# Kernel optimization log

Measured on AMD Instinct MI355X. Metric: run time of the kernel, lower is better.

## Reference

```python
import jax, jax.numpy as jnp
import numpy as np

TEMPLATE0 = 3  # template[0]: prefix prompt length, positions [t0, t0+count) are kept verbatim

def setup_inputs() -> dict:
    key = jax.random.key(0)
    ks = jax.random.split(key, 6)
    B, S, H, E = 16, 512, 768, 19
    scale = 1.0 / np.sqrt(H)
    return {
        "sequence_output": jax.random.normal(ks[0], (B, S, H), jnp.float32),
        "label_init": jax.random.normal(ks[1], (E, H), jnp.float32),
        "attn_w": jax.random.normal(ks[2], (H, H), jnp.float32) * scale,
        "attn_b": jax.random.normal(ks[3], (H,), jnp.float32) * scale,
        "fc_w": jax.random.normal(ks[4], (H,), jnp.float32) * scale,
        "counts": jax.random.randint(ks[5], (B,), 1, 400, jnp.int32),
    }

def reference(sequence_output, label_init, attn_w, attn_b, fc_w, counts):
    # Vectorized form of GPT2SoftmaxForNer_LE.add_label_embedding + attention
    B, S, H = sequence_output.shape
    # attn_linear: torch Linear -> x @ W^T + b
    x_attn = jnp.einsum('bsh,gh->bsg', sequence_output, attn_w) + attn_b  # [B,S,H]
    # att_features = label_embedding + expanded input state; e = tanh(...)
    e = jnp.tanh(x_attn[:, :, None, :] + label_init[None, None, :, :])  # [B,S,E,H]
    scores = jnp.einsum('bseh,h->bse', e, fc_w)  # fc: Linear(H,1,bias=False)
    attn_dist = jax.nn.softmax(scores, axis=-1)
    # (original renormalizes softmax by its sum; sum==1 so it is a no-op)
    ctx = jnp.einsum('bse,eh->bsh', attn_dist, label_init)
    out = ctx + sequence_output  # residual add
    # restore original embeddings at positions [t0, t0 + counts[b])
    pos = jnp.arange(S)[None, :]  # [1,S]
    keep = (pos >= TEMPLATE0) & (pos < counts[:, None] + TEMPLATE0)  # [B,S]
    return jnp.where(keep[:, :, None], sequence_output, out)
```

## Files before the change

### kernel.cpp

```cpp
#include <hip/hip_runtime.h>
#include <hip/hip_fp16.h>

typedef __bf16 bf16_t;
typedef __bf16 bf16x8 __attribute__((ext_vector_type(8)));
typedef _Float16 f16_t;
typedef _Float16 f16x8 __attribute__((ext_vector_type(8)));
typedef float  f32x4  __attribute__((ext_vector_type(4)));

#define B_ 16
#define S_ 512
#define H_ 768
#define E_ 19
#define T0 3
#define ROWS (B_*S_)
#define SCAL 2.8853900817779268f

#define WS_W_OFF  0
#define WS_W_SZ   (H_*H_*2)
#define WS_LS_OFF (WS_W_OFF + WS_W_SZ)
#define WS_LS_SZ  (E_*H_*2)
#define WS_XS_OFF (WS_LS_OFF + WS_LS_SZ)
#define WS_XS_SZ  (ROWS*H_*2)
#define WS_NEED   (WS_XS_OFF + WS_XS_SZ)
#define WS_AB_OFF WS_NEED
#define WS_AB_SZ  (ROWS*H_*2)
#define WS_NEED2  (WS_AB_OFF + WS_AB_SZ)

__device__ __forceinline__ f16_t h_exp2(f16_t x) {
  __half hx = __builtin_bit_cast(__half, x);
  return __builtin_bit_cast(f16_t, hexp2(hx));
}
__device__ __forceinline__ f16_t h_rcp(f16_t x) {
  __half hx = __builtin_bit_cast(__half, x);
  return __builtin_bit_cast(f16_t, hrcp(hx));
}

__global__ __launch_bounds__(256) void prep_kernel(
    const float* __restrict__ w, const float* __restrict__ lab,
    const float* __restrict__ attb, const float* __restrict__ seq,
    bf16_t* __restrict__ wbf, f16_t* __restrict__ lsg, bf16_t* __restrict__ abf) {
  int t = blockIdx.x*256 + threadIdx.x;
  int i = t*8;
  if (i < H_*H_) {
    float4 u = *(const float4*)(w + i);
    float4 v = *(const float4*)(w + i + 4);
    bf16x8 b;
    b[0]=(bf16_t)(u.x*SCAL); b[1]=(bf16_t)(u.y*SCAL); b[2]=(bf16_t)(u.z*SCAL); b[3]=(bf16_t)(u.w*SCAL);
    b[4]=(bf16_t)(v.x*SCAL); b[5]=(bf16_t)(v.y*SCAL); b[6]=(bf16_t)(v.z*SCAL); b[7]=(bf16_t)(v.w*SCAL);
    *(bf16x8*)(wbf + i) = b;
  }
  if (t < E_*H_) {
    int col = t % H_;
    lsg[t] = (f16_t)((lab[t] + attb[col]) * SCAL);
  }
  if (i < ROWS*H_) {
    float4 u = *(const float4*)(seq + i);
    float4 v = *(const float4*)(seq + i + 4);
    bf16x8 b;
    b[0]=(bf16_t)u.x; b[1]=(bf16_t)u.y; b[2]=(bf16_t)u.z; b[3]=(bf16_t)u.w;
    b[4]=(bf16_t)v.x; b[5]=(bf16_t)v.y; b[6]=(bf16_t)v.z; b[7]=(bf16_t)v.w;
    *(bf16x8*)(abf + i) = b;
  }
}

#define G_BM 128
#define G_BN 128
#define G_BK 64
#define G_NT 256
#define G_STEPS (H_/G_BK)

__global__ __launch_bounds__(G_NT, 2) void gemm_xs2(
    const bf16_t* __restrict__ abf, const float* __restrict__ attb,
    const bf16_t* __restrict__ wbf, f16_t* __restrict__ xs) {
  __shared__ __align__(16) unsigned char smem[32768];
  const int tid  = threadIdx.x;
  const int lane = tid & 63, wv = tid >> 6;
  const int bid  = blockIdx.x;
  const int wg   = (bid & 7)*48 + (bid >> 3);
  const int rt   = wg / 6, ct = wg % 6;
  const int arow0 = rt * G_BM;
  const int bcol0 = ct * G_BN;
  const int wr = wv >> 1, wc = wv & 1;
  const int ar = lane & 15, kg = lane >> 4;

  f32x4 acc[4][4] = {};

  auto stage = [&](int s) {
    const int k0 = s * G_BK;
    #pragma unroll
    for (int it = 0; it < 4; ++it) {
      int Lb  = (wv*4 + it) * 1024;
      int L   = Lb + lane*16;
      int row = L >> 7;
      int c   = (L >> 4) & 7;
      int cs  = c ^ (row & 7);
      const bf16_t* srcA = abf + (size_t)(arow0 + row)*H_ + k0 + cs*8;
      __builtin_amdgcn_global_load_lds(
          (const __attribute__((address_space(1))) void*)srcA,
          (__attribute__((address_space(3))) void*)(smem + Lb), 16, 0, 0);
      const bf16_t* srcB = wbf + (size_t)(bcol0 + row)*H_ + k0 + cs*8;
      __builtin_amdgcn_global_load_lds(
          (const __attribute__((address_space(1))) void*)srcB,
          (__attribute__((address_space(3))) void*)(smem + 16384 + Lb), 16, 0, 0);
    }
  };

  stage(0);
  #pragma unroll 1
  for (int s = 0; s < G_STEPS; ++s) {
    __syncthreads();
    #pragma unroll
    for (int ks = 0; ks < 2; ++ks) {
      bf16x8 af[4], bfr[4];
      #pragma unroll
      for (int mf = 0; mf < 4; ++mf) {
        int row = wr*64 + mf*16 + ar;
        int g2  = ks*4 + kg;
        af[mf] = *(const bf16x8*)(smem + row*128 + ((g2 ^ (row & 7)) << 4));
      }
      #pragma unroll
      for (int nf = 0; nf < 4; ++nf) {
        int row = wc*64 + nf*16 + ar;
        int g2  = ks*4 + kg;
        bfr[nf] = *(const bf16x8*)(smem + 16384 + row*128 + ((g2 ^ (row & 7)) << 4));
      }
      #pragma unroll
      for (int mf = 0; mf < 4; ++mf)
        #pragma unroll
        for (int nf = 0; nf < 4; ++nf)
          acc[mf][nf] = __builtin_amdgcn_mfma_f32_16x16x32_bf16(af[mf], bfr[nf], acc[mf][nf], 0,0,0);
    }
    __syncthreads();
    if (s + 1 < G_STEPS) stage(s + 1);
  }

  float bc[4];
  #pragma unroll
  for (int nf = 0; nf < 4; ++nf) bc[nf] = attb[bcol0 + wc*64 + nf*16 + ar] * SCAL;
  #pragma unroll
  for (int mf = 0; mf < 4; ++mf) {
    int rbase = arow0 + wr*64 + mf*16 + kg*4;
    #pragma unroll
    for (int nf = 0; nf < 4; ++nf) {
      int col = bcol0 + wc*64 + nf*16 + ar;
      #pragma unroll
      for (int i = 0; i < 4; ++i)
        xs[(size_t)(rbase + i)*H_ + col] = (f16_t)(acc[mf][nf][i] + bc[nf]);
    }
  }
}

#define K2_R   4
#define K2_PAD 1552
#define K2_SALL (K2_R*K2_PAD)
#define K2_PP   (K2_SALL + K2_R*20*4)
#define K2_LDS  (K2_PP + K2_R*20*4)
__global__ __launch_bounds__(256, 6) void score_ctx(
    const f16_t* __restrict__ xs, const f16_t* __restrict__ lsg,
    const float* __restrict__ fcw, const float* __restrict__ seq,
    const float* __restrict__ lab, const int* __restrict__ counts,
    float* __restrict__ out) {
  __shared__ __align__(16) unsigned char smem[K2_LDS];
  float* Sall = (float*)(smem + K2_SALL);
  float* Pp   = (float*)(smem + K2_PP);
  const int tid = threadIdx.x;
  const int r0  = blockIdx.x * K2_R;

  for (int i = tid; i < K2_R*(H_/8); i += 256) {
    int row = i / (H_/8), kv = i % (H_/8);
    f16x8 v = *(const f16x8*)(xs + (size_t)(r0 + row)*H_ + kv*8);
    *(f16x8*)(smem + row*K2_PAD + kv*16) = v;
  }
  __syncthreads();

  const int g = tid >> 4, k = tid & 15;
  const int r = g & 3, eq = g >> 2;
  const f16_t* xrow = (const f16_t*)(smem + r*K2_PAD + k*96);
  const int ebase = eq*5;
  const f16_t* lbase = lsg + ebase*H_ + k*48;
  const f16_t one = (f16_t)1.0f;

  float s[5] = {};
  #pragma unroll 1
  for (int c = 0; c < 6; ++c) {
    f16x8 xh = *(const f16x8*)(xrow + c*8);
    f32x4 f0 = *(const f32x4*)(fcw + k*48 + c*8);
    f32x4 f1 = *(const f32x4*)(fcw + k*48 + c*8 + 4);
    #pragma unroll
    for (int j = 0; j < 5; ++j) {
      if (j == 4 && eq == 3) continue;
      f16x8 lh = *(const f16x8*)(lbase + j*H_ + c*8);
      f16x8 a  = xh + lh;
      #pragma unroll
      for (int q = 0; q < 8; ++q) {
        f16_t t = h_exp2(a[q]);
        f16_t u = (f16_t)(t + one);
        f16_t rr = h_rcp(u);
        float fq = (q < 4) ? f0[q] : f1[q-4];
        s[j] += fq * (float)rr;
      }
    }
  }
  #pragma unroll
  for (int off = 1; off < 16; off <<= 1)
    #pragma unroll
    for (int j = 0; j < 5; ++j)
      s[j] += __shfl_xor(s[j], off, 64);
  if (k == 0) {
    #pragma unroll
    for (int j = 0; j < 5; ++j) {
      int e = ebase + j;
      if (e < E_) Sall[r*20 + e] = s[j];
    }
  }
  __syncthreads();

  if (tid < K2_R) {
    float s2[E_]; float mx = -1e30f;
    #pragma unroll
    for (int e = 0; e < E_; ++e) {
      float v = -2.0f * Sall[tid*20 + e];
      s2[e] = v; mx = fmaxf(mx, v);
    }
    float ssum = 0.f;
    #pragma unroll
    for (int e = 0; e < E_; ++e) {
      float pr = __builtin_amdgcn_exp2f((s2[e] - mx) * 1.4426950408889634f);
      s2[e] = pr; ssum += pr;
    }
    float rr = __builtin_amdgcn_rcpf(ssum);
    #pragma unroll
    for (int e = 0; e < E_; ++e) Pp[tid*20 + e] = s2[e]*rr;
  }
  __syncthreads();

  if (tid < 192) {
    f32x4 o4[K2_R] = {};
    #pragma unroll 1
    for (int e = 0; e < E_; ++e) {
      f32x4 la = *(const f32x4*)(lab + e*H_ + tid*4);
      #pragma unroll
      for (int rr2 = 0; rr2 < K2_R; ++rr2) {
        float pv = Pp[rr2*20 + e];
        o4[rr2] += pv * la;
      }
    }
    const int batch = r0 >> 9;
    const int cnt = counts[batch];
    #pragma unroll
    for (int rr2 = 0; rr2 < K2_R; ++rr2) {
      int row = r0 + rr2;
      int sp  = row & 511;
      bool keep = (sp >= T0) && (sp < cnt + T0);
      size_t idx = (size_t)row*H_ + tid*4;
      f32x4 sv = *(const f32x4*)(seq + idx);
      f32x4 ov = keep ? sv : (sv + o4[rr2]);
      *(f32x4*)(out + idx) = ov;
    }
  }
}

#define BM 16
#define NW 6
#define NT (NW*64)
#define A_SZ   (BM*H_*2)
#define LS_OFF A_SZ
#define LS_SZ  (E_*H_*2)
#define LDS_SZ (A_SZ + LS_SZ)
#define SP_OFF 0
#define PP_OFF (NW*BM*20*4)

__global__ __launch_bounds__(NT, 3) void ner_fused(
    const float* __restrict__ seq, const float* __restrict__ lab,
    const float* __restrict__ attw, const float* __restrict__ attb,
    const float* __restrict__ fcw, const int* __restrict__ counts,
    float* __restrict__ out)
{
  __shared__ __align__(16) unsigned char smem[LDS_SZ];
  _Float16* Lsh = (_Float16*)(smem + LS_OFF);
  float* Sp = (float*)(smem + SP_OFF);
  float* Pp = (float*)(smem + PP_OFF);
  const int tid   = threadIdx.x;
  const int blk   = blockIdx.x;
  const int batch = blk >> 5;
  const int s0    = (blk & 31) * BM;
  const size_t rowbase = ((size_t)batch * S_ + s0) * H_;
  {
    const float4* src = (const float4*)(seq + rowbase);
    #pragma unroll
    for (int i = 0; i < (BM*H_/8)/NT; ++i) {
      int idx = i*NT + tid;
      int row = idx / (H_/8);
      int kv  = idx % (H_/8);
      float4 u = src[row*(H_/4) + kv*2];
      float4 v = src[row*(H_/4) + kv*2 + 1];
      bf16x8 b;
      b[0]=(bf16_t)u.x; b[1]=(bf16_t)u.y; b[2]=(bf16_t)u.z; b[3]=(bf16_t)u.w;
      b[4]=(bf16_t)v.x; b[5]=(bf16_t)v.y; b[6]=(bf16_t)v.z; b[7]=(bf16_t)v.w;
      int byte = row*(H_*2) + kv*16;
      *(bf16x8*)(smem + (byte ^ ((row & 7) << 4))) = b;
    }
  }
  for (int i = tid*4; i < E_*H_; i += NT*4) {
    int c = i % H_;
    float4 l4 = *(const float4*)(lab + i);
    float4 b4 = *(const float4*)(attb + c);
    int e = i / H_;
    #pragma unroll
    for (int j = 0; j < 4; ++j) {
      int col = c + j;
      int wv2 = col >> 7, rr = col & 127, n = rr >> 4, arr = rr & 15;
      float v = ((&l4.x)[j] + (&b4.x)[j]) * SCAL;
      Lsh[((e*NW + wv2)*16 + arr)*8 + n] = (_Float16)v;
    }
  }
  __syncthreads();
  const int lane = tid & 63;
  const int wv   = tid >> 6;
  const int ar   = lane & 15;
  const int kg   = lane >> 4;
  const int wbase = wv * (H_/NW);
  f32x4 acc[8] = {};
  {
    const int a_sw = (ar & 7) << 4;
    #pragma unroll 1
    for (int step = 0; step < H_/32; ++step) {
      int kb = step*64 + kg*16;
      bf16x8 a0 = *(const bf16x8*)(smem + ((ar*1536 + kb) ^ a_sw));
      int k = step*32 + kg*8;
      #pragma unroll
      for (int n = 0; n < 8; ++n) {
        int gcol = wbase + n*16 + ar;
        float4 u = *(const float4*)(attw + (size_t)gcol*H_ + k);
        float4 v = *(const float4*)(attw + (size_t)gcol*H_ + k + 4);
        bf16x8 bb;
        bb[0]=(bf16_t)(u.x*SCAL); bb[1]=(bf16_t)(u.y*SCAL); bb[2]=(bf16_t)(u.z*SCAL); bb[3]=(bf16_t)(u.w*SCAL);
        bb[4]=(bf16_t)(v.x*SCAL); bb[5]=(bf16_t)(v.y*SCAL); bb[6]=(bf16_t)(v.z*SCAL); bb[7]=(bf16_t)(v.w*SCAL);
        acc[n] = __builtin_amdgcn_mfma_f32_16x16x32_bf16(a0, bb, acc[n], 0,0,0);
      }
    }
  }
  __syncthreads();
  float fcv[8];
  #pragma unroll
  for (int n = 0; n < 8; ++n) fcv[n] = fcw[wbase + n*16 + ar];
  {
    const _Float16* Lw = Lsh + (wv*16 + ar)*8;
    #pragma unroll 1
    for (int e = 0; e < E_; ++e) {
      f16x8 lh = *(const f16x8*)(Lw + e*(NW*128));
      float lv[8];
      #pragma unroll
      for (int n = 0; n < 8; ++n) lv[n] = (float)lh[n];
      float s8[4] = {};
      #pragma unroll
      for (int n = 0; n < 8; ++n)
        #pragma unroll
        for (int i = 0; i < 4; ++i) {
          float t = __builtin_amdgcn_exp2f(acc[n][i] + lv[n]);
          s8[i] += fcv[n] * __builtin_amdgcn_rcpf(t + 1.0f);
        }
      #pragma unroll
      for (int off = 1; off < 16; off <<= 1)
        #pragma unroll
        for (int i = 0; i < 4; ++i)
          s8[i] += __shfl_xor(s8[i], off, 64);
      if (ar == 0) {
        #pragma unroll
        for (int i = 0; i < 4; ++i)
          Sp[(wv*BM + kg*4 + i)*20 + e] = s8[i];
      }
    }
  }
  __syncthreads();
  if (tid % 24 == 0) {
    int row = tid / 24;
    float sc2[E_];
    float mx = -1e30f;
    #pragma unroll
    for (int e = 0; e < E_; ++e) {
      float v = 0.f;
      #pragma unroll
      for (int w2 = 0; w2 < NW; ++w2) v += Sp[(w2*BM + row)*20 + e];
      sc2[e] = -2.0f * v;
      mx = fmaxf(mx, sc2[e]);
    }
    float ssum = 0.f;
    #pragma unroll
    for (int e = 0; e < E_; ++e) {
      float p = __builtin_amdgcn_exp2f((sc2[e] - mx) * 1.4426950408889634f);
      sc2[e] = p; ssum += p;
    }
    float rr = __builtin_amdgcn_rcpf(ssum);
    #pragma unroll
    for (int e = 0; e < E_; ++e) Pp[row*20 + e] = sc2[e]*rr;
  }
  __syncthreads();
  {
    const int cg = tid % 96;
    const int rq = tid / 96;
    float o[4][8] = {};
    const f32x4* L4 = (const f32x4*)lab;
    #pragma unroll 1
    for (int e = 0; e < E_; ++e) {
      f32x4 la = L4[e*(H_/4) + cg*2];
      f32x4 lb = L4[e*(H_/4) + cg*2 + 1];
      #pragma unroll
      for (int rr2 = 0; rr2 < 4; ++rr2) {
        float p = Pp[(rq*4 + rr2)*20 + e];
        o[rr2][0] += p*la[0]; o[rr2][1] += p*la[1]; o[rr2][2] += p*la[2]; o[rr2][3] += p*la[3];
        o[rr2][4] += p*lb[0]; o[rr2][5] += p*lb[1]; o[rr2][6] += p*lb[2]; o[rr2][7] += p*lb[3];
      }
    }
    const int cnt = counts[batch];
    #pragma unroll
    for (int rr2 = 0; rr2 < 4; ++rr2) {
      int row = rq*4 + rr2;
      int sp  = s0 + row;
      bool keep = (sp >= T0) && (sp < cnt + T0);
      size_t idx = rowbase + (size_t)row*H_ + cg*8;
      float4 s1 = *(const float4*)(seq + idx);
      float4 s2v = *(const float4*)(seq + idx + 4);
      float4 o1, o2;
      if (keep) { o1 = s1; o2 = s2v; }
      else {
        o1 = make_float4(s1.x + o[rr2][0], s1.y + o[rr2][1], s1.z + o[rr2][2], s1.w + o[rr2][3]);
        o2 = make_float4(s2v.x + o[rr2][4], s2v.y + o[rr2][5], s2v.z + o[rr2][6], s2v.w + o[rr2][7]);
      }
      *(float4*)(out + idx)     = o1;
      *(float4*)(out + idx + 4) = o2;
    }
  }
}

extern "C" void kernel_launch(void* const* d_in, const int* in_sizes, int n_in,
                              void* d_out, int out_size, void* d_ws, size_t ws_size,
                              hipStream_t stream) {
  const float* seq    = (const float*)d_in[0];
  const float* lab    = (const float*)d_in[1];
  const float* attw   = (const float*)d_in[2];
  const float* attb   = (const float*)d_in[3];
  const float* fcw    = (const float*)d_in[4];
  const int*   counts = (const int*)d_in[5];
  float* out = (float*)d_out;

  if (ws_size >= (size_t)WS_NEED) {
    bf16_t* wbf = (bf16_t*)((char*)d_ws + WS_W_OFF);
    f16_t*  lsg = (f16_t*)((char*)d_ws + WS_LS_OFF);
    f16_t*  xsp = (f16_t*)((char*)d_ws + WS_XS_OFF);
    bf16_t* abf = (ws_size >= (size_t)WS_NEED2)
                ? (bf16_t*)((char*)d_ws + WS_AB_OFF)
                : (bf16_t*)d_out;
    prep_kernel<<<dim3((ROWS*H_/8 + 255)/256), dim3(256), 0, stream>>>(
        attw, lab, attb, seq, wbf, lsg, abf);
    gemm_xs2<<<dim3((ROWS/G_BM)*(H_/G_BN)), dim3(G_NT), 0, stream>>>(
        abf, attb, wbf, xsp);
    score_ctx<<<dim3(ROWS/K2_R), dim3(256), 0, stream>>>(
        xsp, lsg, fcw, seq, lab, counts, out);
  } else {
    ner_fused<<<dim3(ROWS/BM), dim3(NT), 0, stream>>>(seq, lab, attw, attb, fcw, counts, out);
  }
}
```

Before: 63.82 us.

## Factor exp2 across row and label terms to remove per-element exponentials

The code uses exp2(x+l) = exp2(x)*exp2(l). The GEMM epilogue now stores exp2 of the clamped projection, and prep stores exp2 of the clamped label-plus-bias. The score kernel then needs only a packed multiply-add and a reciprocal per element instead of an exp, an add and a reciprocal. The fc weights are converted to f16, and the inner reduction uses fdot2 on packed halves instead of scalar f32 FMAs. The clamping and the f16 products add accuracy risk: tanh is only recovered approximately, and the product can overflow or underflow in f16.

```diff
diff --git a/kernel.cpp b/kernel.cpp
--- a/kernel.cpp
+++ b/kernel.cpp
@@ -4,6 +4,7 @@
 typedef __bf16 bf16_t;
 typedef __bf16 bf16x8 __attribute__((ext_vector_type(8)));
 typedef _Float16 f16_t;
+typedef _Float16 f16x2 __attribute__((ext_vector_type(2)));
 typedef _Float16 f16x8 __attribute__((ext_vector_type(8)));
 typedef float  f32x4  __attribute__((ext_vector_type(4)));
 
@@ -14,31 +15,36 @@
 #define T0 3
 #define ROWS (B_*S_)
 #define SCAL 2.8853900817779268f
+#define ECLAMP_LO (-13.5f)
+#define ECLAMP_HI (15.5f)
 
 #define WS_W_OFF  0
 #define WS_W_SZ   (H_*H_*2)
-#define WS_LS_OFF (WS_W_OFF + WS_W_SZ)
-#define WS_LS_SZ  (E_*H_*2)
-#define WS_XS_OFF (WS_LS_OFF + WS_LS_SZ)
-#define WS_XS_SZ  (ROWS*H_*2)
-#define WS_NEED   (WS_XS_OFF + WS_XS_SZ)
+#define WS_PL_OFF (WS_W_OFF + WS_W_SZ)
+#define WS_PL_SZ  (E_*H_*2)
+#define WS_FC_OFF (WS_PL_OFF + WS_PL_SZ)
+#define WS_FC_SZ  (H_*2)
+#define WS_PX_OFF (WS_FC_OFF + WS_FC_SZ)
+#define WS_PX_SZ  (ROWS*H_*2)
+#define WS_NEED   (WS_PX_OFF + WS_PX_SZ)
 #define WS_AB_OFF WS_NEED
 #define WS_AB_SZ  (ROWS*H_*2)
 #define WS_NEED2  (WS_AB_OFF + WS_AB_SZ)
 
-__device__ __forceinline__ f16_t h_exp2(f16_t x) {
-  __half hx = __builtin_bit_cast(__half, x);
-  return __builtin_bit_cast(f16_t, hexp2(hx));
-}
 __device__ __forceinline__ f16_t h_rcp(f16_t x) {
   __half hx = __builtin_bit_cast(__half, x);
   return __builtin_bit_cast(f16_t, hrcp(hx));
 }
+__device__ __forceinline__ float clamp_e(float v) {
+  return fminf(fmaxf(v, ECLAMP_LO), ECLAMP_HI);
+}
 
 __global__ __launch_bounds__(256) void prep_kernel(
     const float* __restrict__ w, const float* __restrict__ lab,
-    const float* __restrict__ attb, const float* __restrict__ seq,
-    bf16_t* __restrict__ wbf, f16_t* __restrict__ lsg, bf16_t* __restrict__ abf) {
+    const float* __restrict__ attb, const float* __restrict__ fcw,
+    const float* __restrict__ seq,
+    bf16_t* __restrict__ wbf, f16_t* __restrict__ pls,
+    f16_t* __restrict__ fcg, bf16_t* __restrict__ abf) {
   int t = blockIdx.x*256 + threadIdx.x;
   int i = t*8;
   if (i < H_*H_) {
@@ -51,8 +57,10 @@
   }
   if (t < E_*H_) {
     int col = t % H_;
-    lsg[t] = (f16_t)((lab[t] + attb[col]) * SCAL);
-  }
+    float e2 = clamp_e((lab[t] + attb[col]) * SCAL);
+    pls[t] = (f16_t)__builtin_amdgcn_exp2f(e2);
+  }
+  if (t < H_) fcg[t] = (f16_t)fcw[t];
   if (i < ROWS*H_) {
     float4 u = *(const float4*)(seq + i);
     float4 v = *(const float4*)(seq + i + 4);
@@ -70,8 +78,8 @@
 #define G_STEPS (H_/G_BK)
 
 __global__ __launch_bounds__(G_NT, 2) void gemm_xs2(
-    const bf16_t* __restrict__ abf, const float* __restrict__ attb,
-    const bf16_t* __restrict__ wbf, f16_t* __restrict__ xs) {
+    const bf16_t* __restrict__ abf,
+    const bf16_t* __restrict__ wbf, f16_t* __restrict__ px) {
   __shared__ __align__(16) unsigned char smem[32768];
   const int tid  = threadIdx.x;
   const int lane = tid & 63, wv = tid >> 6;
@@ -134,9 +142,6 @@
     if (s + 1 < G_STEPS) stage(s + 1);
   }
 
-  float bc[4];
-  #pragma unroll
-  for (int nf = 0; nf < 4; ++nf) bc[nf] = attb[bcol0 + wc*64 + nf*16 + ar] * SCAL;
   #pragma unroll
   for (int mf = 0; mf < 4; ++mf) {
     int rbase = arow0 + wr*64 + mf*16 + kg*4;
@@ -144,8 +149,10 @@
     for (int nf = 0; nf < 4; ++nf) {
       int col = bcol0 + wc*64 + nf*16 + ar;
       #pragma unroll
-      for (int i = 0; i < 4; ++i)
-        xs[(size_t)(rbase + i)*H_ + col] = (f16_t)(acc[mf][nf][i] + bc[nf]);
+      for (int i = 0; i < 4; ++i) {
+        float v = clamp_e(acc[mf][nf][i]);
+        px[(size_t)(rbase + i)*H_ + col] = (f16_t)__builtin_amdgcn_exp2f(v);
+      }
     }
   }
 }
@@ -156,8 +163,8 @@
 #define K2_PP   (K2_SALL + K2_R*20*4)
 #define K2_LDS  (K2_PP + K2_R*20*4)
 __global__ __launch_bounds__(256, 6) void score_ctx(
-    const f16_t* __restrict__ xs, const f16_t* __restrict__ lsg,
-    const float* __restrict__ fcw, const float* __restrict__ seq,
+    const f16_t* __restrict__ px, const f16_t* __restrict__ pls,
+    const f16_t* __restrict__ fcg, const float* __restrict__ seq,
     const float* __restrict__ lab, const int* __restrict__ counts,
     float* __restrict__ out) {
   __shared__ __align__(16) unsigned char smem[K2_LDS];
@@ -167,8 +174,8 @@
   const int r0  = blockIdx.x * K2_R;
 
   for (int i = tid; i < K2_R*(H_/8); i += 256) {
-    int row = i / (H_/8), kv = i % (H_/8);
-    f16x8 v = *(const f16x8*)(xs + (size_t)(r0 + row)*H_ + kv*8);
+    int row = i / 96, kv = i % 96;
+    f16x8 v = *(const f16x8*)(px + (size_t)(r0 + row)*H_ + kv*8);
     *(f16x8*)(smem + row*K2_PAD + kv*16) = v;
   }
   __syncthreads();
@@ -177,28 +184,28 @@
   const int r = g & 3, eq = g >> 2;
   const f16_t* xrow = (const f16_t*)(smem + r*K2_PAD + k*96);
   const int ebase = eq*5;
-  const f16_t* lbase = lsg + ebase*H_ + k*48;
+  const f16_t* lbase = pls + ebase*H_ + k*48;
   const f16_t one = (f16_t)1.0f;
+  const f16x8 one8 = {one,one,one,one,one,one,one,one};
 
   float s[5] = {};
   #pragma unroll 1
   for (int c = 0; c < 6; ++c) {
-    f16x8 xh = *(const f16x8*)(xrow + c*8);
-    f32x4 f0 = *(const f32x4*)(fcw + k*48 + c*8);
-    f32x4 f1 = *(const f32x4*)(fcw + k*48 + c*8 + 4);
+    f16x8 xh  = *(const f16x8*)(xrow + c*8);
+    f16x8 fch = *(const f16x8*)(fcg + k*48 + c*8);
     #pragma unroll
     for (int j = 0; j < 5; ++j) {
       if (j == 4 && eq == 3) continue;
       f16x8 lh = *(const f16x8*)(lbase + j*H_ + c*8);
-      f16x8 a  = xh + lh;
-      #pragma unroll
-      for (int q = 0; q < 8; ++q) {
-        f16_t t = h_exp2(a[q]);
-        f16_t u = (f16_t)(t + one);
-        f16_t rr = h_rcp(u);
-        float fq = (q < 4) ? f0[q] : f1[q-4];
-        s[j] += fq * (float)rr;
-      }
+      f16x8 u  = xh*lh + one8;
+      f16x8 rr;
+      #pragma unroll
+      for (int q = 0; q < 8; ++q) rr[q] = h_rcp(u[q]);
+      const f16x2* rp = (const f16x2*)&rr;
+      const f16x2* fp = (const f16x2*)&fch;
+      #pragma unroll
+      for (int p = 0; p < 4; ++p)
+        s[j] = __builtin_amdgcn_fdot2(rp[p], fp[p], s[j], false);
     }
   }
   #pragma unroll
@@ -446,17 +453,18 @@
 
   if (ws_size >= (size_t)WS_NEED) {
     bf16_t* wbf = (bf16_t*)((char*)d_ws + WS_W_OFF);
-    f16_t*  lsg = (f16_t*)((char*)d_ws + WS_LS_OFF);
-    f16_t*  xsp = (f16_t*)((char*)d_ws + WS_XS_OFF);
+    f16_t*  pls = (f16_t*)((char*)d_ws + WS_PL_OFF);
+    f16_t*  fcg = (f16_t*)((char*)d_ws + WS_FC_OFF);
+    f16_t*  pxp = (f16_t*)((char*)d_ws + WS_PX_OFF);
     bf16_t* abf = (ws_size >= (size_t)WS_NEED2)
                 ? (bf16_t*)((char*)d_ws + WS_AB_OFF)
                 : (bf16_t*)d_out;
     prep_kernel<<<dim3((ROWS*H_/8 + 255)/256), dim3(256), 0, stream>>>(
-        attw, lab, attb, seq, wbf, lsg, abf);
+        attw, lab, attb, fcw, seq, wbf, pls, fcg, abf);
     gemm_xs2<<<dim3((ROWS/G_BM)*(H_/G_BN)), dim3(G_NT), 0, stream>>>(
-        abf, attb, wbf, xsp);
+        abf, wbf, pxp);
     score_ctx<<<dim3(ROWS/K2_R), dim3(256), 0, stream>>>(
-        xsp, lsg, fcw, seq, lab, counts, out);
+        pxp, pls, fcg, seq, lab, counts, out);
   } else {
     ner_fused<<<dim3(ROWS/BM), dim3(NT), 0, stream>>>(seq, lab, attw, attb, fcw, counts, out);
   }
```

New measurement: 60.18 us. 5.7% less time.
